# Optimization experiments

Measured on AMD Instinct MI355X. Metric: run time of the kernel, lower is better.

The kernel has to match this reference:

```python
import jax, jax.numpy as jnp
import numpy as np

B, S, E, DQ, DV = 8, 2048, 1024, 128, 128


def setup_inputs() -> dict:
    k0 = jax.random.key(0)
    ks = jax.random.split(k0, 10)
    scale_in = 1.0 / np.sqrt(E)
    return {
        "pad_mask": jax.random.uniform(ks[0], (B, S)) < 0.1,  # True = padded key position
        "query": jax.random.normal(ks[1], (B, S, E), jnp.float32),
        "key": jax.random.normal(ks[2], (B, S, E), jnp.float32),
        "value": jax.random.normal(ks[3], (B, S, E), jnp.float32),
        "Wq": jax.random.uniform(ks[4], (E, DQ), jnp.float32, -scale_in, scale_in),
        "bq": jnp.zeros((DQ,), jnp.float32),
        "Wk": jax.random.uniform(ks[5], (E, DQ), jnp.float32, -scale_in, scale_in),
        "bk": jnp.zeros((DQ,), jnp.float32),
        "Wv": jax.random.uniform(ks[6], (E, DV), jnp.float32, -scale_in, scale_in),
        "bv": jnp.zeros((DV,), jnp.float32),
    }


def reference(pad_mask, query, key, value, Wq, bq, Wk, bk, Wv, bv):
    # Linear projections (torch Linear: x @ W^T + b; weights stored pre-transposed here)
    q = query @ Wq + bq  # [B,S,DQ]
    k = key @ Wk + bk    # [B,S,DQ]
    v = value @ Wv + bv  # [B,S,DV]

    scores = jnp.einsum("bqd,bkd->bqk", q, k)  # [B,S,S]
    # Causal mask applied BEFORE scaling (as in source); -inf/scale is still -inf
    seq = scores.shape[1]
    causal = jnp.triu(jnp.ones((seq, seq), bool), k=1)
    scores = jnp.where(causal[None], -jnp.inf, scores)
    scores = scores / jnp.asarray(q.shape[-1] ** 0.5, scores.dtype)
    # Padding mask: mask key positions with -1e9 (broadcast over query dim)
    scores = jnp.where(pad_mask[:, None, :], jnp.asarray(-1e9, scores.dtype), scores)

    attn = jax.nn.softmax(scores, axis=-1)
    return jnp.einsum("bqk,bkd->bqd", attn, v)  # [B,S,DV]
```

## Files before the change

### kernel.cpp

```cpp
#include <hip/hip_runtime.h>
#include <hip/hip_bf16.h>

#define SEQ 2048
#define EMB 1024
#define DH  128
#define QSCALE 0.08838834764831845f

typedef __attribute__((ext_vector_type(4))) float f32x4;
typedef __attribute__((ext_vector_type(8))) short bf16x8;
typedef __attribute__((ext_vector_type(4))) short bf16x4;

__device__ __forceinline__ short f2bf(float f) {
  unsigned u = __builtin_bit_cast(unsigned, f);
  u += 0x7fffu + ((u >> 16) & 1u);
  return (short)(u >> 16);
}

__device__ __forceinline__ float bf2f(short s) {
  unsigned u = ((unsigned)(unsigned short)s) << 16;
  return __builtin_bit_cast(float, u);
}

__device__ __forceinline__ f32x4 mfma16(bf16x8 a, bf16x8 b, f32x4 c) {
  return __builtin_amdgcn_mfma_f32_16x16x32_bf16(a, b, c, 0, 0, 0);
}

__device__ __forceinline__ void gl_lds16(void* lds_base, const void* gsrc) {
  __builtin_amdgcn_global_load_lds(
      (const __attribute__((address_space(1))) void*)gsrc,
      (__attribute__((address_space(3))) void*)lds_base, 16, 0, 0);
}

__global__ void prep_weights(const float* __restrict__ Wq, const float* __restrict__ Wk,
                             const float* __restrict__ Wv, short* __restrict__ wt) {
  int gid = blockIdx.x * 256 + threadIdx.x;
  int lane = gid & 63, c = lane & 15, g = (lane >> 4) & 3;
  int nb = (gid >> 6) & 7;
  int kk = (gid >> 9) & 31;
  int p = gid >> 14;
  const float* W = (p == 0) ? Wq : ((p == 1) ? Wk : Wv);
  bf16x8 v;
#pragma unroll
  for (int j = 0; j < 8; ++j)
    v[j] = f2bf(W[(kk * 32 + g * 8 + j) * DH + nb * 16 + c]);
  *(bf16x8*)(&wt[(size_t)gid * 8]) = v;
}

__global__ __launch_bounds__(64, 2) void proj_gemm(
    const float* __restrict__ Xq, const float* __restrict__ Xk, const float* __restrict__ Xv,
    const short* __restrict__ wt,
    const float* __restrict__ bq, const float* __restrict__ bk, const float* __restrict__ bv,
    short* __restrict__ qp, short* __restrict__ kp, short* __restrict__ vt) {
  __shared__ char abuf[2][4096];
  __shared__ char wbuf[2][8192];

  const int lane = threadIdx.x;
  const int g = lane >> 4, c = lane & 15;
  const int wid = blockIdx.x;
  const int p = wid >> 9, mb = wid & 511;
  const int row0 = mb << 5;
  const float* X    = (p == 0) ? Xq : ((p == 1) ? Xk : Xv);
  const float* bias = (p == 0) ? bq : ((p == 1) ? bk : bv);
  const char* Xb  = (const char*)X;
  const char* Wtb = (const char*)wt + (size_t)p * 262144;

  f32x4 acc[2][8];
#pragma unroll
  for (int rb = 0; rb < 2; ++rb)
#pragma unroll
    for (int nb = 0; nb < 8; ++nb) acc[rb][nb] = (f32x4){0.f, 0.f, 0.f, 0.f};

  auto stage = [&](char* ab, char* wb, int kk) {
#pragma unroll
    for (int i = 0; i < 4; ++i) {
      int q = i * 1024 + lane * 16;
      int lg = q ^ (((q >> 7) & 7) << 4);
      gl_lds16(ab + i * 1024,
               Xb + (size_t)(row0 + (lg >> 7)) * 4096 + kk * 128 + (lg & 127));
    }
#pragma unroll
    for (int i = 0; i < 8; ++i)
      gl_lds16(wb + i * 1024, Wtb + (size_t)kk * 8192 + i * 1024 + lane * 16);
  };

  auto compute = [&](const char* ab, const char* wb) {
    bf16x8 wfr[8];
#pragma unroll
    for (int nb = 0; nb < 8; ++nb)
      wfr[nb] = *(const bf16x8*)(wb + nb * 1024 + lane * 16);
#pragma unroll
    for (int rb = 0; rb < 2; ++rb) {
      int r = (rb << 4) + c;
      int ad = ((r << 7) + (g << 5)) ^ ((r & 7) << 4);
      f32x4 lo = *(const f32x4*)(ab + ad);
      f32x4 hi = *(const f32x4*)(ab + (ad ^ 16));
      bf16x8 a;
#pragma unroll
      for (int j = 0; j < 4; ++j) { a[j] = f2bf(lo[j]); a[4 + j] = f2bf(hi[j]); }
#pragma unroll
      for (int nb = 0; nb < 8; ++nb) acc[rb][nb] = mfma16(a, wfr[nb], acc[rb][nb]);
    }
  };

  stage(abuf[0], wbuf[0], 0);
#pragma unroll 1
  for (int kk = 0; kk < 32; kk += 2) {
    stage(abuf[1], wbuf[1], kk + 1);
    asm volatile("s_waitcnt vmcnt(12)" ::: "memory");
    compute(abuf[0], wbuf[0]);
    __builtin_amdgcn_sched_barrier(0);
    if (kk + 2 < 32) {
      stage(abuf[0], wbuf[0], kk + 2);
      asm volatile("s_waitcnt vmcnt(12)" ::: "memory");
    } else {
      asm volatile("s_waitcnt vmcnt(0)" ::: "memory");
    }
    compute(abuf[1], wbuf[1]);
    __builtin_amdgcn_sched_barrier(0);
  }

  float bvals[8];
#pragma unroll
  for (int nb = 0; nb < 8; ++nb) bvals[nb] = bias[nb * 16 + c];

  if (p < 2) {
    short* outp = (p == 0) ? qp : kp;
    float sc = (p == 0) ? QSCALE : 1.0f;
#pragma unroll
    for (int rb = 0; rb < 2; ++rb)
#pragma unroll
      for (int r = 0; r < 4; ++r) {
        int token = row0 + (rb << 4) + g * 4 + r;
#pragma unroll
        for (int nb = 0; nb < 8; ++nb)
          outp[token * 128 + nb * 16 + c] = f2bf((acc[rb][nb][r] + bvals[nb]) * sc);
      }
  } else {
#pragma unroll
    for (int rb = 0; rb < 2; ++rb) {
      int tok0 = row0 + (rb << 4) + g * 4;
      int b_ = tok0 >> 11, s_ = tok0 & 2047;
#pragma unroll
      for (int nb = 0; nb < 8; ++nb) {
        int col = nb * 16 + c;
        bf16x4 v4;
#pragma unroll
        for (int r = 0; r < 4; ++r) v4[r] = f2bf(acc[rb][nb][r] + bvals[nb]);
        *(bf16x4*)(&vt[((size_t)(b_ * 128 + col)) * 2048 + s_]) = v4;
      }
    }
  }
}

__global__ __launch_bounds__(256) void avgv2_kernel(
    const short* __restrict__ vt, const int* __restrict__ pad,
    const float* __restrict__ bvv, float* __restrict__ avgv) {
  int b = blockIdx.x >> 3, dg = blockIdx.x & 7;
  int t = threadIdx.x, doff = t >> 4, sl = t & 15;
  int d = dg * 16 + doff;
  const short* vrow = vt + ((size_t)(b * 128 + d)) * 2048 + sl * 128;
  const int* prow = pad + (b << 11) + sl * 128;
  float sum = 0.f;
  int cnt = 0;
  for (int i = 0; i < 16; ++i) {
    bf16x8 v8 = *(const bf16x8*)(vrow + i * 8);
#pragma unroll
    for (int j = 0; j < 8; ++j) {
      int pd = prow[i * 8 + j];
      cnt += (pd != 0);
      if (pd) sum += bf2f(v8[j]);
    }
  }
#pragma unroll
  for (int xm = 1; xm < 16; xm <<= 1) {
    sum += __shfl_xor(sum, xm, 64);
    cnt += __shfl_xor(cnt, xm, 64);
  }
  if (sl == 0) avgv[(b << 7) + d] = (cnt > 0) ? (sum / (float)cnt) : 0.f;
  (void)bvv;
}

__device__ __forceinline__ void stage_kv(short* kb, short* vb,
                                         const char* kb_base, const char* vb_base,
                                         int kt, int w, int lane) {
#pragma unroll
  for (int ch = w; ch < 16; ch += 4) {
    int phys = ch * 1024 + lane * 16;
    int lg = phys ^ (((phys >> 8) & 7) << 4);
    gl_lds16((char*)kb + ch * 1024,
             kb_base + (size_t)(kt * 64 + (lg >> 8)) * 256 + (lg & 255));
  }
#pragma unroll
  for (int ch = w; ch < 16; ch += 4) {
    int phys = ch * 1024 + lane * 16;
    int lg = phys ^ (((phys >> 7) & 7) << 4);
    gl_lds16((char*)vb + ch * 1024,
             vb_base + (size_t)(lg >> 7) * 4096 + kt * 128 + (lg & 127));
  }
}

template <bool CAUSAL>
__device__ __forceinline__ void attn_tile(
    const short* __restrict__ k_lds, const short* __restrict__ v_lds, short* __restrict__ p_w,
    const bf16x8 (&qf)[4], f32x4 (&acc_o)[8], float (&m_r)[4], float (&l_r)[4],
    const int* __restrict__ padp, int kt, int qrow_g, int g, int c) {
  f32x4 sc[4];
#pragma unroll
  for (int nb = 0; nb < 4; ++nb) sc[nb] = (f32x4){0.f, 0.f, 0.f, 0.f};
#pragma unroll
  for (int ks = 0; ks < 4; ++ks) {
    bf16x8 kf[4];
#pragma unroll
    for (int nb = 0; nb < 4; ++nb) {
      int n = (nb << 4) + c;
      int off = (n << 8) + (ks << 6) + (g << 4);
      kf[nb] = *(const bf16x8*)((const char*)k_lds + (off ^ ((n & 7) << 4)));
    }
#pragma unroll
    for (int nb = 0; nb < 4; ++nb) sc[nb] = mfma16(qf[ks], kf[nb], sc[nb]);
  }

  int padv[4];
#pragma unroll
  for (int nb = 0; nb < 4; ++nb) padv[nb] = padp[kt + (nb << 4) + c];
  float sv[4][4];
#pragma unroll
  for (int nb = 0; nb < 4; ++nb) {
    bool pd = padv[nb] != 0;
    int key = kt + (nb << 4) + c;
#pragma unroll
    for (int r = 0; r < 4; ++r) {
      float s = sc[nb][r];
      if (CAUSAL && key > qrow_g + r) s = -1e30f;
      if (pd) s = -1e30f;
      sv[nb][r] = s;
    }
  }
  float tmax[4];
#pragma unroll
  for (int r = 0; r < 4; ++r)
    tmax[r] = fmaxf(fmaxf(sv[0][r], sv[1][r]), fmaxf(sv[2][r], sv[3][r]));
#pragma unroll
  for (int xm = 1; xm < 16; xm <<= 1)
#pragma unroll
    for (int r = 0; r < 4; ++r) tmax[r] = fmaxf(tmax[r], __shfl_xor(tmax[r], xm, 64));
  float al[4];
#pragma unroll
  for (int r = 0; r < 4; ++r) {
    float mn = fmaxf(m_r[r], tmax[r]);
    al[r] = __expf(m_r[r] - mn);
    m_r[r] = mn;
  }
  float ls[4] = {0.f, 0.f, 0.f, 0.f};
#pragma unroll
  for (int nb = 0; nb < 4; ++nb)
#pragma unroll
    for (int r = 0; r < 4; ++r) {
      float pp = __expf(sv[nb][r] - m_r[r]);
      sv[nb][r] = pp;
      ls[r] += pp;
    }
#pragma unroll
  for (int xm = 1; xm < 16; xm <<= 1)
#pragma unroll
    for (int r = 0; r < 4; ++r) ls[r] += __shfl_xor(ls[r], xm, 64);
#pragma unroll
  for (int r = 0; r < 4; ++r) l_r[r] = l_r[r] * al[r] + ls[r];
#pragma unroll
  for (int nb = 0; nb < 8; ++nb)
#pragma unroll
    for (int r = 0; r < 4; ++r) acc_o[nb][r] *= al[r];

#pragma unroll
  for (int nb = 0; nb < 4; ++nb)
#pragma unroll
    for (int r = 0; r < 4; ++r)
      p_w[(g * 4 + r) * 72 + (nb << 4) + c] = f2bf(sv[nb][r]);

#pragma unroll
  for (int ks = 0; ks < 2; ++ks) {
    bf16x8 pa = *(const bf16x8*)((const char*)p_w + c * 144 + ks * 64 + g * 16);
#pragma unroll
    for (int nb = 0; nb < 8; ++nb) {
      int n = (nb << 4) + c;
      int off = (n << 7) + (ks << 6) + (g << 4);
      bf16x8 vf = *(const bf16x8*)((const char*)v_lds + (off ^ ((n & 7) << 4)));
      acc_o[nb] = mfma16(pa, vf, acc_o[nb]);
    }
  }
}

__global__ __launch_bounds__(256) void flash_attn(
    const short* __restrict__ qp, const short* __restrict__ kp, const short* __restrict__ vt,
    const int* __restrict__ pad, float* __restrict__ partO, float* __restrict__ partML) {
  __shared__ short k_lds[2][64 * 128];
  __shared__ short v_lds[2][128 * 64];
  __shared__ short p_lds[4][16 * 72];
  const int tid = threadIdx.x, w = tid >> 6, lane = tid & 63;
  const int g = lane >> 4, c = lane & 15;
  const int j = blockIdx.x;
  int b, qi, half;
  if (j < 256) { b = j >> 5; qi = j & 31; half = 0; }
  else { int u = j - 256; b = u >> 5; qi = 31 - (u & 31); half = 1; }
  const int T = qi + 1;
  const int t0 = half ? (T >> 1) : 0;
  const int t1 = half ? T : (T >> 1);
  const int q0 = qi << 6;

  bf16x8 qf[4];
  {
    int token = (b << 11) + q0 + (w << 4) + c;
    const char* qrow = (const char*)qp + (size_t)token * 256;
#pragma unroll
    for (int s = 0; s < 4; ++s) qf[s] = *(const bf16x8*)(qrow + s * 64 + g * 16);
  }
  f32x4 acc_o[8];
#pragma unroll
  for (int i = 0; i < 8; ++i) acc_o[i] = (f32x4){0.f, 0.f, 0.f, 0.f};
  float m_r[4] = {-1e30f, -1e30f, -1e30f, -1e30f};
  float l_r[4] = {0.f, 0.f, 0.f, 0.f};

  const char* kb_base = (const char*)kp + (size_t)(b << 11) * 256;
  const char* vb_base = (const char*)vt + (size_t)b * 524288;
  const int* padp = pad + (b << 11);
  const int qrow_g = q0 + (w << 4) + (g << 2);

  if (t1 > t0) {
    stage_kv(k_lds[0], v_lds[0], kb_base, vb_base, t0, w, lane);
    __syncthreads();
    int cur = 0;
    for (int t = t0; t < t1; ++t) {
      if (t + 1 < t1)
        stage_kv(k_lds[cur ^ 1], v_lds[cur ^ 1], kb_base, vb_base, t + 1, w, lane);
      if (half && t == T - 1)
        attn_tile<true>(k_lds[cur], v_lds[cur], p_lds[w], qf, acc_o, m_r, l_r,
                        padp, t << 6, qrow_g, g, c);
      else
        attn_tile<false>(k_lds[cur], v_lds[cur], p_lds[w], qf, acc_o, m_r, l_r,
                         padp, t << 6, qrow_g, g, c);
      __syncthreads();
      cur ^= 1;
    }
  }

  float* pO = partO + (size_t)j * (64 * 128);
  float* pML = partML + (size_t)j * 128;
#pragma unroll
  for (int nb = 0; nb < 8; ++nb)
#pragma unroll
    for (int r = 0; r < 4; ++r)
      pO[(w * 16 + g * 4 + r) * 128 + (nb << 4) + c] = acc_o[nb][r];
  if (c == 0)
#pragma unroll
    for (int r = 0; r < 4; ++r) {
      pML[(w * 16 + g * 4 + r) * 2] = m_r[r];
      pML[(w * 16 + g * 4 + r) * 2 + 1] = l_r[r];
    }
}

__global__ __launch_bounds__(256) void combine_kernel(
    const float* __restrict__ partO, const float* __restrict__ partML,
    const float* __restrict__ avgv, float* __restrict__ out) {
  int gid = blockIdx.x * 256 + threadIdx.x;
  int row = gid >> 5;
  int d4 = gid & 31;
  int b = row >> 11, s = row & 2047;
  int qt = s >> 6, lr = s & 63;
  int wid1 = (b << 5) + qt;
  int wid2 = 256 + (b << 5) + (31 - qt);
  float m1 = partML[wid1 * 128 + lr * 2], l1 = partML[wid1 * 128 + lr * 2 + 1];
  float m2 = partML[wid2 * 128 + lr * 2], l2 = partML[wid2 * 128 + lr * 2 + 1];
  float m = fmaxf(m1, m2);
  f32x4 o;
  if (m < -1e8f) {
    o = *(const f32x4*)(avgv + (b << 7) + (d4 << 2));
  } else {
    float f1 = __expf(m1 - m), f2 = __expf(m2 - m);
    float inv = 1.0f / (l1 * f1 + l2 * f2);
    f32x4 o1 = *(const f32x4*)(partO + ((size_t)wid1 * 64 + lr) * 128 + (d4 << 2));
    f32x4 o2 = *(const f32x4*)(partO + ((size_t)wid2 * 64 + lr) * 128 + (d4 << 2));
#pragma unroll
    for (int k = 0; k < 4; ++k) o[k] = (o1[k] * f1 + o2[k] * f2) * inv;
  }
  *(f32x4*)(out + (size_t)row * 128 + (d4 << 2)) = o;
}

extern "C" void kernel_launch(void* const* d_in, const int* in_sizes, int n_in,
                              void* d_out, int out_size, void* d_ws, size_t ws_size,
                              hipStream_t stream) {
  const int*   pad   = (const int*)d_in[0];
  const float* query = (const float*)d_in[1];
  const float* key   = (const float*)d_in[2];
  const float* value = (const float*)d_in[3];
  const float* Wq    = (const float*)d_in[4];
  const float* bq    = (const float*)d_in[5];
  const float* Wk    = (const float*)d_in[6];
  const float* bk    = (const float*)d_in[7];
  const float* Wv    = (const float*)d_in[8];
  const float* bv    = (const float*)d_in[9];
  char* ws = (char*)d_ws;
  short* wt    = (short*)ws;
  short* qp    = (short*)(ws + 786432);
  short* kp    = (short*)(ws + 4980736);
  short* vt    = (short*)(ws + 9175040);
  float* partO = (float*)(ws + 13369344);
  float* partML= (float*)(ws + 30146560);
  float* avgv  = (float*)(ws + 30408704);
  float* out   = (float*)d_out;

  prep_weights<<<dim3(192), dim3(256), 0, stream>>>(Wq, Wk, Wv, wt);
  proj_gemm<<<dim3(1536), dim3(64), 0, stream>>>(query, key, value, wt, bq, bk, bv, qp, kp, vt);
  avgv2_kernel<<<dim3(64), dim3(256), 0, stream>>>(vt, pad, bv, avgv);
  flash_attn<<<dim3(512), dim3(256), 0, stream>>>(qp, kp, vt, pad, partO, partML);
  combine_kernel<<<dim3(2048), dim3(256), 0, stream>>>(partO, partML, avgv, out);
}
```

Before: 97.60 us.

## Load projection weights directly to registers with triple-buffered prefetch, larger A stages

```diff
diff --git a/kernel.cpp b/kernel.cpp
--- a/kernel.cpp
+++ b/kernel.cpp
@@ -51,8 +51,8 @@
     const short* __restrict__ wt,
     const float* __restrict__ bq, const float* __restrict__ bk, const float* __restrict__ bv,
     short* __restrict__ qp, short* __restrict__ kp, short* __restrict__ vt) {
-  __shared__ char abuf[2][4096];
-  __shared__ char wbuf[2][8192];
+  __shared__ f32x4 a_lds4[2][1024];
+  char* a_lds = (char*)a_lds4;
 
   const int lane = threadIdx.x;
   const int g = lane >> 4, c = lane & 15;
@@ -62,7 +62,7 @@
   const float* X    = (p == 0) ? Xq : ((p == 1) ? Xk : Xv);
   const float* bias = (p == 0) ? bq : ((p == 1) ? bk : bv);
   const char* Xb  = (const char*)X;
-  const char* Wtb = (const char*)wt + (size_t)p * 262144;
+  const char* WT  = (const char*)wt + (size_t)p * 262144;
 
   f32x4 acc[2][8];
 #pragma unroll
@@ -70,52 +70,60 @@
 #pragma unroll
     for (int nb = 0; nb < 8; ++nb) acc[rb][nb] = (f32x4){0.f, 0.f, 0.f, 0.f};
 
-  auto stage = [&](char* ab, char* wb, int kk) {
-#pragma unroll
-    for (int i = 0; i < 4; ++i) {
-      int q = i * 1024 + lane * 16;
-      int lg = q ^ (((q >> 7) & 7) << 4);
-      gl_lds16(ab + i * 1024,
-               Xb + (size_t)(row0 + (lg >> 7)) * 4096 + kk * 128 + (lg & 127));
-    }
-#pragma unroll
-    for (int i = 0; i < 8; ++i)
-      gl_lds16(wb + i * 1024, Wtb + (size_t)kk * 8192 + i * 1024 + lane * 16);
+  bf16x8 wr[3][8];
+
+  auto stage_A = [&](int slot, int kc) {
+#pragma unroll
+    for (int j = 0; j < 16; ++j) {
+      int phys = j * 1024 + lane * 16;
+      int row = phys >> 9;
+      int off = phys & 511;
+      gl_lds16(a_lds + slot * 16384 + j * 1024,
+               Xb + (size_t)(row0 + row) * 4096 + kc * 512 + (off ^ ((row & 7) << 4)));
+    }
   };
 
-  auto compute = [&](const char* ab, const char* wb) {
-    bf16x8 wfr[8];
+  auto loadW = [&](bf16x8* dst, int t) {
 #pragma unroll
     for (int nb = 0; nb < 8; ++nb)
-      wfr[nb] = *(const bf16x8*)(wb + nb * 1024 + lane * 16);
+      dst[nb] = *(const bf16x8*)(WT + (size_t)t * 8192 + nb * 1024 + lane * 16);
+  };
+
+  auto compute = [&](const bf16x8* wf, int t) {
+    int slot = (t >> 2) & 1, s = t & 3;
+    const char* ab = a_lds + slot * 16384;
 #pragma unroll
     for (int rb = 0; rb < 2; ++rb) {
       int r = (rb << 4) + c;
-      int ad = ((r << 7) + (g << 5)) ^ ((r & 7) << 4);
+      int ad = (r << 9) + (((s << 7) + (g << 5)) ^ ((r & 7) << 4));
       f32x4 lo = *(const f32x4*)(ab + ad);
       f32x4 hi = *(const f32x4*)(ab + (ad ^ 16));
       bf16x8 a;
 #pragma unroll
       for (int j = 0; j < 4; ++j) { a[j] = f2bf(lo[j]); a[4 + j] = f2bf(hi[j]); }
 #pragma unroll
-      for (int nb = 0; nb < 8; ++nb) acc[rb][nb] = mfma16(a, wfr[nb], acc[rb][nb]);
+      for (int nb = 0; nb < 8; ++nb) acc[rb][nb] = mfma16(a, wf[nb], acc[rb][nb]);
     }
   };
 
-  stage(abuf[0], wbuf[0], 0);
-#pragma unroll 1
-  for (int kk = 0; kk < 32; kk += 2) {
-    stage(abuf[1], wbuf[1], kk + 1);
-    asm volatile("s_waitcnt vmcnt(12)" ::: "memory");
-    compute(abuf[0], wbuf[0]);
+  stage_A(0, 0);
+  loadW(wr[0], 0);
+  loadW(wr[1], 1);
+  __builtin_amdgcn_sched_barrier(0);
+
+#pragma unroll
+  for (int t = 0; t < 32; ++t) {
+    if ((t & 3) == 2 && t < 28)
+      stage_A(((t >> 2) + 1) & 1, (t >> 2) + 1);
+    if (t + 2 < 32)
+      loadW(wr[(t + 2) % 3], t + 2);
     __builtin_amdgcn_sched_barrier(0);
-    if (kk + 2 < 32) {
-      stage(abuf[0], wbuf[0], kk + 2);
-      asm volatile("s_waitcnt vmcnt(12)" ::: "memory");
-    } else {
-      asm volatile("s_waitcnt vmcnt(0)" ::: "memory");
-    }
-    compute(abuf[1], wbuf[1]);
+    if (t == 31)                         asm volatile("s_waitcnt vmcnt(0)" ::: "memory");
+    else if (t == 30)                    asm volatile("s_waitcnt vmcnt(8)" ::: "memory");
+    else if ((t & 3) >= 2 && t < 28)     asm volatile("s_waitcnt vmcnt(32)" ::: "memory");
+    else                                 asm volatile("s_waitcnt vmcnt(16)" ::: "memory");
+    __builtin_amdgcn_sched_barrier(0);
+    compute(wr[t % 3], t);
     __builtin_amdgcn_sched_barrier(0);
   }
 
```

After: 106.1 us. 8.7% more time.
